# Optimization experiments

Measured on AMD Instinct MI355X. Metric: run time of the kernel, lower is better.

Reference implementation:

```python
import jax, jax.numpy as jnp
import numpy as np

N, D, C, E, K = 100000, 64, 40, 1600000, 2

def setup_inputs() -> dict:
    key = jax.random.key(0)
    k1, k2, k3 = jax.random.split(key, 3)
    x = jax.random.normal(k1, (N, D), dtype=jnp.float32)
    edge_index = jax.random.randint(k2, (2, E), 0, N, dtype=jnp.int64)
    W = jax.random.normal(k3, (D, C), dtype=jnp.float32) * 0.05
    b = jnp.zeros((C,), dtype=jnp.float32)
    return {"x": x, "edge_index": edge_index, "W": W, "b": b}

def reference(x, edge_index, W, b):
    n = x.shape[0]
    self_loop = jnp.arange(n, dtype=edge_index.dtype)
    row = jnp.concatenate([edge_index[0], self_loop])  # [E+N]
    col = jnp.concatenate([edge_index[1], self_loop])  # [E+N]
    # degree over row (out-degree incl. self loops), as in torch_geometric.utils.degree
    deg = jax.ops.segment_sum(jnp.ones_like(row, dtype=x.dtype), row, num_segments=n)
    deg_inv_sqrt = jnp.where(deg > 0, jax.lax.rsqrt(deg), 0.0)
    norm = deg_inv_sqrt[row] * deg_inv_sqrt[col]  # [E+N]
    # K hops of SpMM: out[r] += norm_e * x[c] for each edge e=(r,c)
    for _ in range(K):
        x = jax.ops.segment_sum(norm[:, None] * x[col], row, num_segments=n)
    logits = x @ W + b  # [N, C]
    return jax.nn.log_softmax(logits, axis=1)
```

## Files before the change

### kernel.cpp

```cpp
#include <hip/hip_runtime.h>
#include <math.h>


#define D_FEAT 64
#define NCLS 40
#define BROWS 512
#define BROWS_LOG 9
#define BINCAP 10240
#define CSRCAP 12288
#define EPT 10

__device__ __forceinline__ unsigned pack_bf16_2(float lo, float hi) {
    unsigned ulo = __float_as_uint(lo);
    unsigned uhi = __float_as_uint(hi);
    ulo = (ulo + 0x7fffu + ((ulo >> 16) & 1u)) >> 16;
    uhi = (uhi + 0x7fffu + ((uhi >> 16) & 1u)) & 0xffff0000u;
    return uhi | ulo;
}

__device__ __forceinline__ void acc2(unsigned u, float& a, float& b) {
    a += __uint_as_float(u << 16);
    b += __uint_as_float(u & 0xffff0000u);
}

__global__ void zero_cursors_kernel(int* __restrict__ cur, int nb) {
    int i = blockIdx.x * blockDim.x + threadIdx.x;
    if (i < nb) cur[i] = 0;
}

__global__ __launch_bounds__(256) void bin_edges_kernel(const int* __restrict__ rows,
                                                        const int* __restrict__ cols,
                                                        int* __restrict__ bucket_cursor,
                                                        unsigned* __restrict__ bins,
                                                        int e, int nb) {
    __shared__ int cnt[512];
    for (int i = threadIdx.x; i < nb; i += 256) cnt[i] = 0;
    __syncthreads();
    int base = blockIdx.x * (256 * EPT) + threadIdx.x;
    int rr[EPT], cc[EPT];
#pragma unroll
    for (int k = 0; k < EPT; k++) {
        int idx = base + k * 256;
        if (idx < e) { rr[k] = rows[idx]; cc[k] = cols[idx]; }
        else { rr[k] = -1; cc[k] = 0; }
    }
#pragma unroll
    for (int k = 0; k < EPT; k++)
        if (rr[k] >= 0) atomicAdd(&cnt[rr[k] >> BROWS_LOG], 1);
    __syncthreads();
    for (int i = threadIdx.x; i < nb; i += 256) {
        int c = cnt[i];
        cnt[i] = (c > 0) ? atomicAdd(&bucket_cursor[i], c) : 0;
    }
    __syncthreads();
#pragma unroll
    for (int k = 0; k < EPT; k++) {
        if (rr[k] >= 0) {
            int b = rr[k] >> BROWS_LOG;
            int pos = atomicAdd(&cnt[b], 1);
            bins[(size_t)b * BINCAP + pos] =
                ((unsigned)(rr[k] & (BROWS - 1)) << 17) | (unsigned)cc[k];
        }
    }
}

__global__ __launch_bounds__(512) void build_csr_kernel(const unsigned* __restrict__ bins,
                                                        const int* __restrict__ bucket_cursor,
                                                        int* __restrict__ csr_col,
                                                        uint2* __restrict__ row_info,
                                                        float* __restrict__ dis, int n) {
    __shared__ int cnt[512];
    __shared__ int sm[512];
    __shared__ int cur[512];
    __shared__ int lcsr[CSRCAP];
    int b = blockIdx.x;
    int tid = threadIdx.x;
    int m = bucket_cursor[b];
    cnt[tid] = 0;
    __syncthreads();
    const unsigned* bp = bins + (size_t)b * BINCAP;
    for (int i = tid; i < m; i += 512) atomicAdd(&cnt[bp[i] >> 17], 1);
    __syncthreads();
    int c = cnt[tid];
    int padded = (c + 3) & ~3;
    int r = b * BROWS + tid;
    if (r < n) dis[r] = rsqrtf(1.0f + (float)c);
    sm[tid] = padded;
    __syncthreads();
    for (int off = 1; off < 512; off <<= 1) {
        int t = (tid >= off) ? sm[tid - off] : 0;
        __syncthreads();
        sm[tid] += t;
        __syncthreads();
    }
    int off0 = sm[tid] - padded;
    cur[tid] = off0;
    if (r < n) row_info[r] = make_uint2((unsigned)(b * CSRCAP + off0), (unsigned)padded);
    __syncthreads();
    for (int i = tid; i < m; i += 512) {
        unsigned u = bp[i];
        int pos = atomicAdd(&cur[u >> 17], 1);
        lcsr[pos] = (int)(u & 0x1FFFFu);
    }
    __syncthreads();
    for (int i2 = off0 + 1; i2 < off0 + c; i2++) {
        int key = lcsr[i2];
        int j = i2 - 1;
        while (j >= off0 && lcsr[j] > key) { lcsr[j + 1] = lcsr[j]; j--; }
        lcsr[j + 1] = key;
    }
    for (int j = off0 + c; j < off0 + padded; j++) lcsr[j] = n;
    __syncthreads();
    int tot = sm[511];
    int* cp = csr_col + (size_t)b * CSRCAP;
    for (int i = tid; i < tot; i += 512) cp[i] = lcsr[i];
}

__global__ void scale_x_kernel(const float* __restrict__ x, const float* __restrict__ dis,
                               unsigned* __restrict__ xs0, unsigned* __restrict__ xs1, int n) {
    int i = blockIdx.x * blockDim.x + threadIdx.x;
    int total = (n + 1) * (D_FEAT / 2);
    if (i >= total) return;
    int node = i >> 5;
    if (node < n) {
        float s = dis[node];
        float2 v = ((const float2*)x)[i];
        xs0[i] = pack_bf16_2(s * v.x, s * v.y);
    } else {
        xs0[i] = 0u;
        xs1[i] = 0u;
    }
}

__global__ __launch_bounds__(256) void spmm_hop1_kernel(const uint2* __restrict__ xs_in,
                                                        uint2* __restrict__ xs_out,
                                                        const uint2* __restrict__ row_info,
                                                        const int* __restrict__ csr_col,
                                                        const float* __restrict__ dis, int n) {
    int wave = (blockIdx.x * blockDim.x + threadIdx.x) >> 6;
    int lane = threadIdx.x & 63;
    int q = lane >> 4, ql = lane & 15;
    int r = wave * 4 + q;
    bool valid = r < n;
    int s = 0, len = 0;
    if (valid) { uint2 info = row_info[r]; s = (int)info.x; len = (int)info.y; }
    int maxlen = len;
    maxlen = max(maxlen, __shfl_xor(maxlen, 16, 64));
    maxlen = max(maxlen, __shfl_xor(maxlen, 32, 64));

    float h0 = 0.f, h1 = 0.f, h2 = 0.f, h3 = 0.f;
    const uint4* cp = (const uint4*)(csr_col + s);
    for (int base = 0; base < maxlen; base += 8) {
        uint2 u0 = make_uint2(0u, 0u), u1 = u0, u2 = u0, u3 = u0;
        uint2 u4 = u0, u5 = u0, u6 = u0, u7 = u0;
        if (base < len) {
            uint4 cv = cp[base >> 2];
            u0 = xs_in[cv.x * 16 + ql];
            u1 = xs_in[cv.y * 16 + ql];
            u2 = xs_in[cv.z * 16 + ql];
            u3 = xs_in[cv.w * 16 + ql];
        }
        if (base + 4 < len) {
            uint4 cv = cp[(base >> 2) + 1];
            u4 = xs_in[cv.x * 16 + ql];
            u5 = xs_in[cv.y * 16 + ql];
            u6 = xs_in[cv.z * 16 + ql];
            u7 = xs_in[cv.w * 16 + ql];
        }
        acc2(u0.x, h0, h1); acc2(u0.y, h2, h3);
        acc2(u1.x, h0, h1); acc2(u1.y, h2, h3);
        acc2(u2.x, h0, h1); acc2(u2.y, h2, h3);
        acc2(u3.x, h0, h1); acc2(u3.y, h2, h3);
        acc2(u4.x, h0, h1); acc2(u4.y, h2, h3);
        acc2(u5.x, h0, h1); acc2(u5.y, h2, h3);
        acc2(u6.x, h0, h1); acc2(u6.y, h2, h3);
        acc2(u7.x, h0, h1); acc2(u7.y, h2, h3);
    }
    if (valid) {
        uint2 us = xs_in[r * 16 + ql];
        acc2(us.x, h0, h1); acc2(us.y, h2, h3);
        float dr = dis[r];
        float dr2 = dr * dr;
        xs_out[r * 16 + ql] = make_uint2(pack_bf16_2(dr2 * h0, dr2 * h1),
                                         pack_bf16_2(dr2 * h2, dr2 * h3));
    }
}

__global__ __launch_bounds__(256) void spmm_logits_kernel(const uint2* __restrict__ xs_in,
                                                          const uint2* __restrict__ row_info,
                                                          const int* __restrict__ csr_col,
                                                          const float* __restrict__ dis,
                                                          const float* __restrict__ W,
                                                          const float* __restrict__ b,
                                                          float* __restrict__ out, int n) {
    __shared__ float Wl[D_FEAT * NCLS];
    __shared__ float bl[NCLS];
    for (int i = threadIdx.x; i < D_FEAT * NCLS; i += blockDim.x) Wl[i] = W[i];
    for (int i = threadIdx.x; i < NCLS; i += blockDim.x) bl[i] = b[i];
    __syncthreads();

    int wave = (blockIdx.x * blockDim.x + threadIdx.x) >> 6;
    int lane = threadIdx.x & 63;
    int q = lane >> 4, ql = lane & 15;
    int r = wave * 4 + q;
    bool valid = r < n;
    int s = 0, len = 0;
    if (valid) { uint2 info = row_info[r]; s = (int)info.x; len = (int)info.y; }
    int maxlen = len;
    maxlen = max(maxlen, __shfl_xor(maxlen, 16, 64));
    maxlen = max(maxlen, __shfl_xor(maxlen, 32, 64));

    float h0 = 0.f, h1 = 0.f, h2 = 0.f, h3 = 0.f;
    const uint4* cp = (const uint4*)(csr_col + s);
    for (int base = 0; base < maxlen; base += 8) {
        uint2 u0 = make_uint2(0u, 0u), u1 = u0, u2 = u0, u3 = u0;
        uint2 u4 = u0, u5 = u0, u6 = u0, u7 = u0;
        if (base < len) {
            uint4 cv = cp[base >> 2];
            u0 = xs_in[cv.x * 16 + ql];
            u1 = xs_in[cv.y * 16 + ql];
            u2 = xs_in[cv.z * 16 + ql];
            u3 = xs_in[cv.w * 16 + ql];
        }
        if (base + 4 < len) {
            uint4 cv = cp[(base >> 2) + 1];
            u4 = xs_in[cv.x * 16 + ql];
            u5 = xs_in[cv.y * 16 + ql];
            u6 = xs_in[cv.z * 16 + ql];
            u7 = xs_in[cv.w * 16 + ql];
        }
        acc2(u0.x, h0, h1); acc2(u0.y, h2, h3);
        acc2(u1.x, h0, h1); acc2(u1.y, h2, h3);
        acc2(u2.x, h0, h1); acc2(u2.y, h2, h3);
        acc2(u3.x, h0, h1); acc2(u3.y, h2, h3);
        acc2(u4.x, h0, h1); acc2(u4.y, h2, h3);
        acc2(u5.x, h0, h1); acc2(u5.y, h2, h3);
        acc2(u6.x, h0, h1); acc2(u6.y, h2, h3);
        acc2(u7.x, h0, h1); acc2(u7.y, h2, h3);
    }

    float y0, y1, y2;
    {
        uint2 us = valid ? xs_in[r * 16 + ql] : make_uint2(0u, 0u);
        acc2(us.x, h0, h1); acc2(us.y, h2, h3);
        float dr = valid ? dis[r] : 0.f;
        h0 *= dr; h1 *= dr; h2 *= dr; h3 *= dr;

        int c0 = ql, c1 = ql + 16;
        int c2 = (ql < 8) ? (ql + 32) : ql;
        y0 = bl[c0]; y1 = bl[c1]; y2 = bl[c2];
        int qbase = q << 4;
#pragma unroll
        for (int d = 0; d < D_FEAT; d++) {
            int src = qbase + (d >> 2);
            float xv;
            switch (d & 3) {
                case 0: xv = __shfl(h0, src, 64); break;
                case 1: xv = __shfl(h1, src, 64); break;
                case 2: xv = __shfl(h2, src, 64); break;
                default: xv = __shfl(h3, src, 64); break;
            }
            y0 += xv * Wl[d * NCLS + c0];
            y1 += xv * Wl[d * NCLS + c1];
            y2 += xv * Wl[d * NCLS + c2];
        }
    }

    bool has3 = (ql < 8);
    float m = fmaxf(y0, y1);
    if (has3) m = fmaxf(m, y2);
#pragma unroll
    for (int o = 8; o > 0; o >>= 1) m = fmaxf(m, __shfl_xor(m, o, 64));
    float sm = __expf(y0 - m) + __expf(y1 - m) + (has3 ? __expf(y2 - m) : 0.f);
#pragma unroll
    for (int o = 8; o > 0; o >>= 1) sm += __shfl_xor(sm, o, 64);
    float lse = m + __logf(sm);

    if (valid) {
        float* op = out + (long long)r * NCLS;
        op[ql] = y0 - lse;
        op[ql + 16] = y1 - lse;
        if (has3) op[ql + 32] = y2 - lse;
    }
}

extern "C" void kernel_launch(void* const* d_in, const int* in_sizes, int n_in,
                              void* d_out, int out_size, void* d_ws, size_t ws_size,
                              hipStream_t stream) {
    const float* x  = (const float*)d_in[0];
    const int*   ei = (const int*)d_in[1];
    const float* W  = (const float*)d_in[2];
    const float* b  = (const float*)d_in[3];
    float* out = (float*)d_out;

    const int n = in_sizes[0] / D_FEAT;
    const int e = in_sizes[1] / 2;
    const int nb = (n + BROWS - 1) / BROWS;

    const int* rows = ei;
    const int* cols = ei + e;

    size_t na = ((size_t)n + 256) & ~(size_t)255;
    int*      bucket_cursor = (int*)d_ws;
    float*    dis           = (float*)(bucket_cursor + 256);
    uint2*    row_info      = (uint2*)(dis + na);
    unsigned* bins          = (unsigned*)(row_info + na);
    int*      csr_col       = (int*)(bins + (size_t)nb * BINCAP);
    unsigned* xs0           = (unsigned*)(csr_col + (size_t)nb * CSRCAP);
    unsigned* xs1           = xs0 + (size_t)(n + 1) * (D_FEAT / 2);

    const int BS = 256;

    zero_cursors_kernel<<<1, 256, 0, stream>>>(bucket_cursor, nb);
    {
        int blocks = (e + BS * EPT - 1) / (BS * EPT);
        bin_edges_kernel<<<blocks, BS, 0, stream>>>(rows, cols, bucket_cursor, bins, e, nb);
    }
    build_csr_kernel<<<nb, 512, 0, stream>>>(bins, bucket_cursor, csr_col, row_info, dis, n);
    {
        int tot = (n + 1) * (D_FEAT / 2);
        scale_x_kernel<<<(tot + BS - 1) / BS, BS, 0, stream>>>(x, dis, xs0, xs1, n);
    }

    int nwaves = (n + 3) / 4;
    int blocks = (nwaves * 64 + BS - 1) / BS;
    spmm_hop1_kernel<<<blocks, BS, 0, stream>>>((const uint2*)xs0, (uint2*)xs1,
                                                row_info, csr_col, dis, n);
    spmm_logits_kernel<<<blocks, BS, 0, stream>>>((const uint2*)xs1, row_info, csr_col,
                                                  dis, W, b, out, n);
}
```

Before: 253.0 us.

## Split CSR rows into column-range chunks and interleave row groups per wave

Each row's neighbor list is partitioned into four column-range chunks, and each wave processes four row groups, sweeping chunk k across all groups before moving to the next chunk. Neighbor gathers at any moment therefore concentrate on one quarter of the feature table, improving L2 locality. Bucket size is halved to 256 rows with 256-thread CSR build blocks, more edges per thread are binned, and the CSR copy-out uses int4 stores. In exchange there is more chunk padding, more register pressure from four accumulator sets, and per-chunk lengths packed into 8 bits, which assumes fewer than 256 neighbors per chunk.

```diff
diff --git a/kernel.cpp b/kernel.cpp
--- a/kernel.cpp
+++ b/kernel.cpp
@@ -4,11 +4,13 @@
 
 #define D_FEAT 64
 #define NCLS 40
-#define BROWS 512
-#define BROWS_LOG 9
-#define BINCAP 10240
-#define CSRCAP 12288
-#define EPT 10
+#define BROWS 256
+#define BROWS_LOG 8
+#define BINCAP 4608
+#define CSRCAP 7680
+#define EPT 25
+#define NCHUNK 4
+#define WGROUPS 4
 
 __device__ __forceinline__ unsigned pack_bf16_2(float lo, float hi) {
     unsigned ulo = __float_as_uint(lo);
@@ -64,56 +66,79 @@
     }
 }
 
-__global__ __launch_bounds__(512) void build_csr_kernel(const unsigned* __restrict__ bins,
+__global__ __launch_bounds__(256) void build_csr_kernel(const unsigned* __restrict__ bins,
                                                         const int* __restrict__ bucket_cursor,
                                                         int* __restrict__ csr_col,
-                                                        uint2* __restrict__ row_info,
-                                                        float* __restrict__ dis, int n) {
-    __shared__ int cnt[512];
-    __shared__ int sm[512];
-    __shared__ int cur[512];
+                                                        uint2* __restrict__ vinfo,
+                                                        float* __restrict__ dis,
+                                                        int n, int q1) {
+    __shared__ int cnt[BROWS * NCHUNK];
+    __shared__ int cur[BROWS * NCHUNK];
+    __shared__ int sm[BROWS];
     __shared__ int lcsr[CSRCAP];
     int b = blockIdx.x;
     int tid = threadIdx.x;
     int m = bucket_cursor[b];
-    cnt[tid] = 0;
+    const int q2 = 2 * q1, q3 = 3 * q1;
+    for (int i = tid; i < BROWS * NCHUNK; i += 256) cnt[i] = 0;
     __syncthreads();
     const unsigned* bp = bins + (size_t)b * BINCAP;
-    for (int i = tid; i < m; i += 512) atomicAdd(&cnt[bp[i] >> 17], 1);
-    __syncthreads();
-    int c = cnt[tid];
-    int padded = (c + 3) & ~3;
+    for (int i = tid; i < m; i += 256) {
+        unsigned u = bp[i];
+        int col = (int)(u & 0x1FFFFu);
+        int ch = (col >= q2) ? ((col >= q3) ? 3 : 2) : ((col >= q1) ? 1 : 0);
+        atomicAdd(&cnt[(u >> 17) * NCHUNK + ch], 1);
+    }
+    __syncthreads();
+    int c0 = cnt[tid * 4 + 0], c1 = cnt[tid * 4 + 1];
+    int c2 = cnt[tid * 4 + 2], c3 = cnt[tid * 4 + 3];
+    int p0 = (c0 + 3) & ~3, p1 = (c1 + 3) & ~3, p2 = (c2 + 3) & ~3, p3 = (c3 + 3) & ~3;
+    int T = p0 + p1 + p2 + p3;
     int r = b * BROWS + tid;
-    if (r < n) dis[r] = rsqrtf(1.0f + (float)c);
-    sm[tid] = padded;
-    __syncthreads();
-    for (int off = 1; off < 512; off <<= 1) {
+    if (r < n) dis[r] = rsqrtf(1.0f + (float)(c0 + c1 + c2 + c3));
+    sm[tid] = T;
+    __syncthreads();
+    for (int off = 1; off < 256; off <<= 1) {
         int t = (tid >= off) ? sm[tid - off] : 0;
         __syncthreads();
         sm[tid] += t;
         __syncthreads();
     }
-    int off0 = sm[tid] - padded;
-    cur[tid] = off0;
-    if (r < n) row_info[r] = make_uint2((unsigned)(b * CSRCAP + off0), (unsigned)padded);
-    __syncthreads();
-    for (int i = tid; i < m; i += 512) {
+    int off0 = sm[tid] - T;
+    int s0 = off0, s1 = s0 + p0, s2 = s1 + p1, s3 = s2 + p2;
+    cur[tid * 4 + 0] = s0; cur[tid * 4 + 1] = s1;
+    cur[tid * 4 + 2] = s2; cur[tid * 4 + 3] = s3;
+    if (r < n)
+        vinfo[r] = make_uint2((unsigned)(b * CSRCAP + off0),
+                              (unsigned)(p0 | (p1 << 8) | (p2 << 16) | (p3 << 24)));
+    __syncthreads();
+    for (int i = tid; i < m; i += 256) {
         unsigned u = bp[i];
-        int pos = atomicAdd(&cur[u >> 17], 1);
-        lcsr[pos] = (int)(u & 0x1FFFFu);
-    }
-    __syncthreads();
-    for (int i2 = off0 + 1; i2 < off0 + c; i2++) {
-        int key = lcsr[i2];
-        int j = i2 - 1;
-        while (j >= off0 && lcsr[j] > key) { lcsr[j + 1] = lcsr[j]; j--; }
-        lcsr[j + 1] = key;
-    }
-    for (int j = off0 + c; j < off0 + padded; j++) lcsr[j] = n;
-    __syncthreads();
-    int tot = sm[511];
-    int* cp = csr_col + (size_t)b * CSRCAP;
-    for (int i = tid; i < tot; i += 512) cp[i] = lcsr[i];
+        int col = (int)(u & 0x1FFFFu);
+        int ch = (col >= q2) ? ((col >= q3) ? 3 : 2) : ((col >= q1) ? 1 : 0);
+        int pos = atomicAdd(&cur[(u >> 17) * NCHUNK + ch], 1);
+        lcsr[pos] = col;
+    }
+    __syncthreads();
+    int st[4] = {s0, s1, s2, s3};
+    int cc[4] = {c0, c1, c2, c3};
+    int pp[4] = {p0, p1, p2, p3};
+#pragma unroll
+    for (int k = 0; k < 4; k++) {
+        int base = st[k], c = cc[k], p = pp[k];
+        for (int i2 = base + 1; i2 < base + c; i2++) {
+            int key = lcsr[i2];
+            int j = i2 - 1;
+            while (j >= base && lcsr[j] > key) { lcsr[j + 1] = lcsr[j]; j--; }
+            lcsr[j + 1] = key;
+        }
+        for (int j = base + c; j < base + p; j++) lcsr[j] = n;
+    }
+    __syncthreads();
+    int tot = sm[255];
+    int4* cp4 = (int4*)(csr_col + (size_t)b * CSRCAP);
+    const int4* l4 = (const int4*)lcsr;
+    for (int i = tid; i < (tot >> 2); i += 256) cp4[i] = l4[i];
 }
 
 __global__ void scale_x_kernel(const float* __restrict__ x, const float* __restrict__ dis,
@@ -132,115 +157,125 @@
     }
 }
 
+__device__ __forceinline__ void gather8(const uint4* __restrict__ cp,
+                                        const uint2* __restrict__ xs, int ql,
+                                        int base, int plen,
+                                        float& h0, float& h1, float& h2, float& h3) {
+    uint4 cv = cp[base >> 2];
+    uint2 u0 = xs[cv.x * 16 + ql];
+    uint2 u1 = xs[cv.y * 16 + ql];
+    uint2 u2 = xs[cv.z * 16 + ql];
+    uint2 u3 = xs[cv.w * 16 + ql];
+    uint2 u4 = make_uint2(0u, 0u), u5 = u4, u6 = u4, u7 = u4;
+    if (base + 4 < plen) {
+        uint4 cv2 = cp[(base >> 2) + 1];
+        u4 = xs[cv2.x * 16 + ql];
+        u5 = xs[cv2.y * 16 + ql];
+        u6 = xs[cv2.z * 16 + ql];
+        u7 = xs[cv2.w * 16 + ql];
+    }
+    acc2(u0.x, h0, h1); acc2(u0.y, h2, h3);
+    acc2(u1.x, h0, h1); acc2(u1.y, h2, h3);
+    acc2(u2.x, h0, h1); acc2(u2.y, h2, h3);
+    acc2(u3.x, h0, h1); acc2(u3.y, h2, h3);
+    acc2(u4.x, h0, h1); acc2(u4.y, h2, h3);
+    acc2(u5.x, h0, h1); acc2(u5.y, h2, h3);
+    acc2(u6.x, h0, h1); acc2(u6.y, h2, h3);
+    acc2(u7.x, h0, h1); acc2(u7.y, h2, h3);
+}
+
 __global__ __launch_bounds__(256) void spmm_hop1_kernel(const uint2* __restrict__ xs_in,
                                                         uint2* __restrict__ xs_out,
-                                                        const uint2* __restrict__ row_info,
+                                                        const uint2* __restrict__ vinfo,
                                                         const int* __restrict__ csr_col,
-                                                        const float* __restrict__ dis, int n) {
-    int wave = (blockIdx.x * blockDim.x + threadIdx.x) >> 6;
+                                                        const float* __restrict__ dis,
+                                                        int n, int gstride) {
+    int w = blockIdx.x * 4 + (threadIdx.x >> 6);
     int lane = threadIdx.x & 63;
     int q = lane >> 4, ql = lane & 15;
-    int r = wave * 4 + q;
-    bool valid = r < n;
-    int s = 0, len = 0;
-    if (valid) { uint2 info = row_info[r]; s = (int)info.x; len = (int)info.y; }
-    int maxlen = len;
-    maxlen = max(maxlen, __shfl_xor(maxlen, 16, 64));
-    maxlen = max(maxlen, __shfl_xor(maxlen, 32, 64));
-
-    float h0 = 0.f, h1 = 0.f, h2 = 0.f, h3 = 0.f;
-    const uint4* cp = (const uint4*)(csr_col + s);
-    for (int base = 0; base < maxlen; base += 8) {
-        uint2 u0 = make_uint2(0u, 0u), u1 = u0, u2 = u0, u3 = u0;
-        uint2 u4 = u0, u5 = u0, u6 = u0, u7 = u0;
-        if (base < len) {
-            uint4 cv = cp[base >> 2];
-            u0 = xs_in[cv.x * 16 + ql];
-            u1 = xs_in[cv.y * 16 + ql];
-            u2 = xs_in[cv.z * 16 + ql];
-            u3 = xs_in[cv.w * 16 + ql];
-        }
-        if (base + 4 < len) {
-            uint4 cv = cp[(base >> 2) + 1];
-            u4 = xs_in[cv.x * 16 + ql];
-            u5 = xs_in[cv.y * 16 + ql];
-            u6 = xs_in[cv.z * 16 + ql];
-            u7 = xs_in[cv.w * 16 + ql];
-        }
-        acc2(u0.x, h0, h1); acc2(u0.y, h2, h3);
-        acc2(u1.x, h0, h1); acc2(u1.y, h2, h3);
-        acc2(u2.x, h0, h1); acc2(u2.y, h2, h3);
-        acc2(u3.x, h0, h1); acc2(u3.y, h2, h3);
-        acc2(u4.x, h0, h1); acc2(u4.y, h2, h3);
-        acc2(u5.x, h0, h1); acc2(u5.y, h2, h3);
-        acc2(u6.x, h0, h1); acc2(u6.y, h2, h3);
-        acc2(u7.x, h0, h1); acc2(u7.y, h2, h3);
-    }
-    if (valid) {
-        uint2 us = xs_in[r * 16 + ql];
-        acc2(us.x, h0, h1); acc2(us.y, h2, h3);
-        float dr = dis[r];
-        float dr2 = dr * dr;
-        xs_out[r * 16 + ql] = make_uint2(pack_bf16_2(dr2 * h0, dr2 * h1),
-                                         pack_bf16_2(dr2 * h2, dr2 * h3));
+
+    int rr[WGROUPS]; int cs[WGROUPS]; unsigned pl[WGROUPS];
+    float h[WGROUPS][4];
+#pragma unroll
+    for (int g = 0; g < WGROUPS; g++) {
+        int rg = g * gstride + w;
+        int r = rg * 4 + q;
+        rr[g] = r;
+        if (r < n) { uint2 iv = vinfo[r]; cs[g] = (int)iv.x; pl[g] = iv.y; }
+        else { cs[g] = 0; pl[g] = 0u; }
+        h[g][0] = h[g][1] = h[g][2] = h[g][3] = 0.f;
+    }
+#pragma unroll
+    for (int k = 0; k < NCHUNK; k++) {
+#pragma unroll
+        for (int g = 0; g < WGROUPS; g++) {
+            int plen = (int)((pl[g] >> (8 * k)) & 0xFFu);
+            const uint4* cp = (const uint4*)(csr_col + cs[g]);
+            for (int base = 0; base < plen; base += 8)
+                gather8(cp, xs_in, ql, base, plen, h[g][0], h[g][1], h[g][2], h[g][3]);
+            cs[g] += plen;
+        }
+    }
+#pragma unroll
+    for (int g = 0; g < WGROUPS; g++) {
+        int r = rr[g];
+        if (r < n) {
+            uint2 us = xs_in[r * 16 + ql];
+            acc2(us.x, h[g][0], h[g][1]); acc2(us.y, h[g][2], h[g][3]);
+            float dr = dis[r];
+            float dr2 = dr * dr;
+            xs_out[r * 16 + ql] = make_uint2(pack_bf16_2(dr2 * h[g][0], dr2 * h[g][1]),
+                                             pack_bf16_2(dr2 * h[g][2], dr2 * h[g][3]));
+        }
     }
 }
 
 __global__ __launch_bounds__(256) void spmm_logits_kernel(const uint2* __restrict__ xs_in,
-                                                          const uint2* __restrict__ row_info,
+                                                          const uint2* __restrict__ vinfo,
                                                           const int* __restrict__ csr_col,
                                                           const float* __restrict__ dis,
                                                           const float* __restrict__ W,
                                                           const float* __restrict__ b,
-                                                          float* __restrict__ out, int n) {
+                                                          float* __restrict__ out,
+                                                          int n, int gstride) {
     __shared__ float Wl[D_FEAT * NCLS];
     __shared__ float bl[NCLS];
     for (int i = threadIdx.x; i < D_FEAT * NCLS; i += blockDim.x) Wl[i] = W[i];
     for (int i = threadIdx.x; i < NCLS; i += blockDim.x) bl[i] = b[i];
     __syncthreads();
 
-    int wave = (blockIdx.x * blockDim.x + threadIdx.x) >> 6;
+    int w = blockIdx.x * 4 + (threadIdx.x >> 6);
     int lane = threadIdx.x & 63;
     int q = lane >> 4, ql = lane & 15;
-    int r = wave * 4 + q;
-    bool valid = r < n;
-    int s = 0, len = 0;
-    if (valid) { uint2 info = row_info[r]; s = (int)info.x; len = (int)info.y; }
-    int maxlen = len;
-    maxlen = max(maxlen, __shfl_xor(maxlen, 16, 64));
-    maxlen = max(maxlen, __shfl_xor(maxlen, 32, 64));
-
-    float h0 = 0.f, h1 = 0.f, h2 = 0.f, h3 = 0.f;
-    const uint4* cp = (const uint4*)(csr_col + s);
-    for (int base = 0; base < maxlen; base += 8) {
-        uint2 u0 = make_uint2(0u, 0u), u1 = u0, u2 = u0, u3 = u0;
-        uint2 u4 = u0, u5 = u0, u6 = u0, u7 = u0;
-        if (base < len) {
-            uint4 cv = cp[base >> 2];
-            u0 = xs_in[cv.x * 16 + ql];
-            u1 = xs_in[cv.y * 16 + ql];
-            u2 = xs_in[cv.z * 16 + ql];
-            u3 = xs_in[cv.w * 16 + ql];
-        }
-        if (base + 4 < len) {
-            uint4 cv = cp[(base >> 2) + 1];
-            u4 = xs_in[cv.x * 16 + ql];
-            u5 = xs_in[cv.y * 16 + ql];
-            u6 = xs_in[cv.z * 16 + ql];
-            u7 = xs_in[cv.w * 16 + ql];
-        }
-        acc2(u0.x, h0, h1); acc2(u0.y, h2, h3);
-        acc2(u1.x, h0, h1); acc2(u1.y, h2, h3);
-        acc2(u2.x, h0, h1); acc2(u2.y, h2, h3);
-        acc2(u3.x, h0, h1); acc2(u3.y, h2, h3);
-        acc2(u4.x, h0, h1); acc2(u4.y, h2, h3);
-        acc2(u5.x, h0, h1); acc2(u5.y, h2, h3);
-        acc2(u6.x, h0, h1); acc2(u6.y, h2, h3);
-        acc2(u7.x, h0, h1); acc2(u7.y, h2, h3);
-    }
-
-    float y0, y1, y2;
-    {
+
+    int rr[WGROUPS]; int cs[WGROUPS]; unsigned pl[WGROUPS];
+    float h[WGROUPS][4];
+#pragma unroll
+    for (int g = 0; g < WGROUPS; g++) {
+        int rg = g * gstride + w;
+        int r = rg * 4 + q;
+        rr[g] = r;
+        if (r < n) { uint2 iv = vinfo[r]; cs[g] = (int)iv.x; pl[g] = iv.y; }
+        else { cs[g] = 0; pl[g] = 0u; }
+        h[g][0] = h[g][1] = h[g][2] = h[g][3] = 0.f;
+    }
+#pragma unroll
+    for (int k = 0; k < NCHUNK; k++) {
+#pragma unroll
+        for (int g = 0; g < WGROUPS; g++) {
+            int plen = (int)((pl[g] >> (8 * k)) & 0xFFu);
+            const uint4* cp = (const uint4*)(csr_col + cs[g]);
+            for (int base = 0; base < plen; base += 8)
+                gather8(cp, xs_in, ql, base, plen, h[g][0], h[g][1], h[g][2], h[g][3]);
+            cs[g] += plen;
+        }
+    }
+
+#pragma unroll
+    for (int g = 0; g < WGROUPS; g++) {
+        int r = rr[g];
+        bool valid = r < n;
+        float h0 = h[g][0], h1 = h[g][1], h2 = h[g][2], h3 = h[g][3];
         uint2 us = valid ? xs_in[r * 16 + ql] : make_uint2(0u, 0u);
         acc2(us.x, h0, h1); acc2(us.y, h2, h3);
         float dr = valid ? dis[r] : 0.f;
@@ -248,7 +283,7 @@
 
         int c0 = ql, c1 = ql + 16;
         int c2 = (ql < 8) ? (ql + 32) : ql;
-        y0 = bl[c0]; y1 = bl[c1]; y2 = bl[c2];
+        float y0 = bl[c0], y1 = bl[c1], y2 = bl[c2];
         int qbase = q << 4;
 #pragma unroll
         for (int d = 0; d < D_FEAT; d++) {
@@ -264,23 +299,23 @@
             y1 += xv * Wl[d * NCLS + c1];
             y2 += xv * Wl[d * NCLS + c2];
         }
-    }
-
-    bool has3 = (ql < 8);
-    float m = fmaxf(y0, y1);
-    if (has3) m = fmaxf(m, y2);
-#pragma unroll
-    for (int o = 8; o > 0; o >>= 1) m = fmaxf(m, __shfl_xor(m, o, 64));
-    float sm = __expf(y0 - m) + __expf(y1 - m) + (has3 ? __expf(y2 - m) : 0.f);
-#pragma unroll
-    for (int o = 8; o > 0; o >>= 1) sm += __shfl_xor(sm, o, 64);
-    float lse = m + __logf(sm);
-
-    if (valid) {
-        float* op = out + (long long)r * NCLS;
-        op[ql] = y0 - lse;
-        op[ql + 16] = y1 - lse;
-        if (has3) op[ql + 32] = y2 - lse;
+
+        bool has3 = (ql < 8);
+        float m = fmaxf(y0, y1);
+        if (has3) m = fmaxf(m, y2);
+#pragma unroll
+        for (int o = 8; o > 0; o >>= 1) m = fmaxf(m, __shfl_xor(m, o, 64));
+        float sm = __expf(y0 - m) + __expf(y1 - m) + (has3 ? __expf(y2 - m) : 0.f);
+#pragma unroll
+        for (int o = 8; o > 0; o >>= 1) sm += __shfl_xor(sm, o, 64);
+        float lse = m + __logf(sm);
+
+        if (valid) {
+            float* op = out + (long long)r * NCLS;
+            op[ql] = y0 - lse;
+            op[ql + 16] = y1 - lse;
+            if (has3) op[ql + 32] = y2 - lse;
+        }
     }
 }
 
@@ -296,36 +331,38 @@
     const int n = in_sizes[0] / D_FEAT;
     const int e = in_sizes[1] / 2;
     const int nb = (n + BROWS - 1) / BROWS;
+    const int q1 = (n + NCHUNK - 1) / NCHUNK;
 
     const int* rows = ei;
     const int* cols = ei + e;
 
     size_t na = ((size_t)n + 256) & ~(size_t)255;
     int*      bucket_cursor = (int*)d_ws;
-    float*    dis           = (float*)(bucket_cursor + 256);
-    uint2*    row_info      = (uint2*)(dis + na);
-    unsigned* bins          = (unsigned*)(row_info + na);
+    float*    dis           = (float*)(bucket_cursor + 512);
+    uint2*    vinfo         = (uint2*)(dis + na);
+    unsigned* bins          = (unsigned*)(vinfo + na);
     int*      csr_col       = (int*)(bins + (size_t)nb * BINCAP);
     unsigned* xs0           = (unsigned*)(csr_col + (size_t)nb * CSRCAP);
     unsigned* xs1           = xs0 + (size_t)(n + 1) * (D_FEAT / 2);
 
     const int BS = 256;
 
-    zero_cursors_kernel<<<1, 256, 0, stream>>>(bucket_cursor, nb);
+    zero_cursors_kernel<<<2, 256, 0, stream>>>(bucket_cursor, nb);
     {
         int blocks = (e + BS * EPT - 1) / (BS * EPT);
         bin_edges_kernel<<<blocks, BS, 0, stream>>>(rows, cols, bucket_cursor, bins, e, nb);
     }
-    build_csr_kernel<<<nb, 512, 0, stream>>>(bins, bucket_cursor, csr_col, row_info, dis, n);
+    build_csr_kernel<<<nb, BS, 0, stream>>>(bins, bucket_cursor, csr_col, vinfo, dis, n, q1);
     {
         int tot = (n + 1) * (D_FEAT / 2);
         scale_x_kernel<<<(tot + BS - 1) / BS, BS, 0, stream>>>(x, dis, xs0, xs1, n);
     }
 
     int nwaves = (n + 3) / 4;
-    int blocks = (nwaves * 64 + BS - 1) / BS;
+    int gstride = (nwaves + WGROUPS - 1) / WGROUPS;
+    int blocks = (gstride * 64 + BS - 1) / BS;
     spmm_hop1_kernel<<<blocks, BS, 0, stream>>>((const uint2*)xs0, (uint2*)xs1,
-                                                row_info, csr_col, dis, n);
-    spmm_logits_kernel<<<blocks, BS, 0, stream>>>((const uint2*)xs1, row_info, csr_col,
-                                                  dis, W, b, out, n);
-}
+                                                vinfo, csr_col, dis, n, gstride);
+    spmm_logits_kernel<<<blocks, BS, 0, stream>>>((const uint2*)xs1, vinfo, csr_col,
+                                                  dis, W, b, out, n, gstride);
+}
```

New measurement: 276.5 us. 9.3% more time.
